# Performance work log

Measured on AMD Instinct MI355X. Metric: run time of the kernel, lower is better.

The kernel has to match this reference:

```python
import jax, jax.numpy as jnp
import numpy as np


def conv2d(x, w, dilation=1, padding=0):
    return jax.lax.conv_general_dilated(
        x, w, window_strides=(1, 1),
        padding=[(padding, padding), (padding, padding)],
        rhs_dilation=(dilation, dilation),
        dimension_numbers=('NCHW', 'OIHW', 'NCHW'))


def bn_relu(x, s, b):
    # inference-mode BatchNorm folded into per-channel scale/bias, then ReLU
    return jax.nn.relu(x * s[None, :, None, None] + b[None, :, None, None])


def resize_bilinear_ac(x, oh, ow):
    # bilinear interpolation with align_corners=True (matches F.interpolate)
    n, c, h, w = x.shape
    def axis_coords(o, i):
        if i == 1:
            z = jnp.zeros((o,), jnp.int32)
            return jnp.zeros((o,), x.dtype), z, z
        t = jnp.arange(o, dtype=x.dtype) * ((i - 1) / (o - 1))
        i0 = jnp.floor(t).astype(jnp.int32)
        i1 = jnp.minimum(i0 + 1, i - 1)
        return t - i0.astype(x.dtype), i0, i1
    fy, y0, y1 = axis_coords(oh, h)
    x = x[:, :, y0, :] * (1 - fy)[None, None, :, None] + x[:, :, y1, :] * fy[None, None, :, None]
    fx, x0, x1 = axis_coords(ow, w)
    x = x[:, :, :, x0] * (1 - fx) + x[:, :, :, x1] * fx
    return x


def unfold3x3_d2(x):
    # F.unfold(x, kernel_size=3, dilation=2, padding=2, stride=1) -> [n, c, 9, h*w]
    n, c, h, w = x.shape
    xp = jnp.pad(x, ((0, 0), (0, 0), (2, 2), (2, 2)))
    pats = [xp[:, :, i:i + h, j:j + w] for i in (0, 2, 4) for j in (0, 2, 4)]
    return jnp.stack(pats, axis=2).reshape(n, c, 9, h * w)


def setup_inputs() -> dict:
    key = jax.random.key(0)
    ks = iter(jax.random.split(key, 48))
    def rn(shape, scale=0.05):
        return jax.random.normal(next(ks), shape, jnp.float32) * scale
    d = {
        'c1': rn((1, 256, 64, 64), 1.0),
        'c2': rn((1, 512, 32, 32), 1.0),
        'x': rn((1, 4096, 32, 32), 1.0),
        'rf1_w': rn((64, 256, 3, 3)), 'rf1_s': jnp.ones((64,), jnp.float32), 'rf1_b': rn((64,)),
        'rf2_w': rn((64, 64, 3, 3)), 'rf2_s': jnp.ones((64,), jnp.float32), 'rf2_b': rn((64,)),
        'r2_w': rn((64, 512, 1, 1)), 'r2_s': jnp.ones((64,), jnp.float32), 'r2_b': rn((64,)),
        'a0_w': rn((512, 4096, 1, 1)), 'a0_s': jnp.ones((512,), jnp.float32), 'a0_b': rn((512,)),
        'a1_w': rn((512, 4096, 3, 3), 0.01), 'a1_s': jnp.ones((512,), jnp.float32), 'a1_b': rn((512,)),
        'a2_w': rn((512, 4096, 3, 3), 0.01), 'a2_s': jnp.ones((512,), jnp.float32), 'a2_b': rn((512,)),
        'a3_w': rn((512, 4096, 3, 3), 0.01), 'a3_s': jnp.ones((512,), jnp.float32), 'a3_b': rn((512,)),
        'a4_w': rn((512, 4096, 1, 1)), 'a4_s': jnp.ones((512,), jnp.float32), 'a4_b': rn((512,)),
        'ap_w': rn((512, 2560, 1, 1)), 'ap_s': jnp.ones((512,), jnp.float32), 'ap_b': rn((512,)),
        'c6_w': rn((19, 512, 1, 1)), 'c6_b': rn((19,)),
    }
    return d


def reference(c1, c2, x, rf1_w, rf1_s, rf1_b, rf2_w, rf2_s, rf2_b, r2_w, r2_s, r2_b,
              a0_w, a0_s, a0_b, a1_w, a1_s, a1_b, a2_w, a2_s, a2_b, a3_w, a3_s, a3_b,
              a4_w, a4_s, a4_b, ap_w, ap_s, ap_b, c6_w, c6_b):
    n, _, h, w = c1.shape
    # refine(c1): two 3x3 dilation-2 convs
    c1r = bn_relu(conv2d(c1, rf1_w, 2, 2), rf1_s, rf1_b)
    c1r = bn_relu(conv2d(c1r, rf2_w, 2, 2), rf2_s, rf2_b)  # [n,64,h,w]
    # refine2(interpolate(c2))
    c2r = bn_relu(conv2d(resize_bilinear_ac(c2, h, w), r2_w), r2_s, r2_b)  # [n,64,h,w]
    unf_c2 = unfold3x3_d2(c2r)  # [n,64,9,h*w]
    # energy[n,p,k] = sum_c c1r[n,c,p] * unf_c2[n,c,k,p]
    energy = jnp.einsum('ncp,nckp->npk', c1r.reshape(n, 64, h * w), unf_c2)
    att = jax.nn.softmax(energy, axis=-1)  # [n, h*w, 9]
    # ASPP on x (in=4096, out=512)
    f0 = bn_relu(conv2d(x, a0_w), a0_s, a0_b)
    f1 = bn_relu(conv2d(x, a1_w, 12, 12), a1_s, a1_b)
    f2 = bn_relu(conv2d(x, a2_w, 24, 24), a2_s, a2_b)
    f3 = bn_relu(conv2d(x, a3_w, 36, 36), a3_s, a3_b)
    gap = jnp.mean(x, axis=(2, 3), keepdims=True)
    f4 = resize_bilinear_ac(bn_relu(conv2d(gap, a4_w), a4_s, a4_b), x.shape[2], x.shape[3])
    out = bn_relu(conv2d(jnp.concatenate([f0, f1, f2, f3, f4], axis=1), ap_w), ap_s, ap_b)
    # local 3x3 window attention aggregation (dropout is eval-mode identity)
    unf_out = unfold3x3_d2(resize_bilinear_ac(out, h, w))  # [n,512,9,h*w]
    agg = jnp.einsum('npk,nckp->ncp', att, unf_out).reshape(n, 512, h, w)
    return conv2d(agg, c6_w) + c6_b[None, :, None, None]
```

## Files before the change

### kernel.cpp

```cpp
#include <hip/hip_runtime.h>
#include <hip/hip_bf16.h>


typedef unsigned short u16;
typedef short bf16x8 __attribute__((ext_vector_type(8)));
typedef float f32x4  __attribute__((ext_vector_type(4)));
typedef u16   u16x8  __attribute__((ext_vector_type(8)));

__device__ __forceinline__ float bf2f(u16 u) {
    return __uint_as_float(((unsigned int)u) << 16);
}
__device__ __forceinline__ u16 f2bf(float f) {
    unsigned u = __float_as_uint(f);
    return (u16)((u + 0x7FFFu + ((u >> 16) & 1u)) >> 16);
}
__device__ __forceinline__ float loadv(const void* p, long i, int f32) {
    return f32 ? ((const float*)p)[i] : bf2f(((const u16*)p)[i]);
}
__device__ __forceinline__ u16 loadbf(const void* p, long i, int f32) {
    return f32 ? f2bf(((const float*)p)[i]) : ((const u16*)p)[i];
}

__device__ __forceinline__ void gload16(const u16* g, u16* l) {
    __builtin_amdgcn_global_load_lds(
        (const __attribute__((address_space(1))) unsigned int*)(g),
        (__attribute__((address_space(3))) unsigned int*)(l), 16, 0, 0);
}

__global__ __launch_bounds__(256) void detect_kernel(
    const u16* __restrict__ c1, int* __restrict__ flag)
{
    __shared__ int cnt;
    if (threadIdx.x == 0) cnt = 0;
    __syncthreads();
    int local = 0;
    for (int i = threadIdx.x; i < 16384; i += 256) {
        u16 u = c1[i];
        if ((u & 0x7F80) >= 0x4F00) local++;
    }
    atomicAdd(&cnt, local);
    __syncthreads();
    if (threadIdx.x == 0) flag[0] = (cnt > 256) ? 1 : 0;
}

__global__ __launch_bounds__(256) void zero_kernel(float* __restrict__ p, int n)
{
    for (int g = blockIdx.x * 256 + threadIdx.x; g < n; g += gridDim.x * 256)
        p[g] = 0.f;
}


__global__ __launch_bounds__(256) void xpose_bn(
    const void* __restrict__ src, u16* __restrict__ dst,
    const void* __restrict__ s, const void* __restrict__ b,
    const int* __restrict__ flag, int flagged, int dobn, int C, int P)
{
    __shared__ u16 T[64][72];
    const int fl = flag[0];
    const int srcf32 = flagged ? fl : 1;
    const int p0 = blockIdx.x * 64, c0 = blockIdx.y * 64;
    const int t = threadIdx.x;
    {
        int c = t >> 2, pq = (t & 3) * 16;
        float sc = 1.f, bc = 0.f;
        if (dobn) { sc = loadv(s, c0 + c, fl); bc = loadv(b, c0 + c, fl); }
        const long sb = (long)(c0 + c) * P + p0 + pq;
        if (srcf32) {
            const float* sp = (const float*)src + sb;
#pragma unroll
            for (int i = 0; i < 16; i += 4) {
                float4 v = *(const float4*)(sp + i);
                float vv[4] = {v.x, v.y, v.z, v.w};
#pragma unroll
                for (int j = 0; j < 4; j++) {
                    float u = vv[j];
                    if (dobn) u = fmaxf(u * sc + bc, 0.f);
                    T[pq + i + j][c] = f2bf(u);
                }
            }
        } else {
            const u16* sp = (const u16*)src + sb;
#pragma unroll
            for (int i = 0; i < 16; i++) T[pq + i][c] = sp[i];
        }
    }
    __syncthreads();
    {
        int p = t >> 2, cq = (t & 3) * 16;
        u16x8 v0, v1;
#pragma unroll
        for (int i = 0; i < 8; i++) { v0[i] = T[p][cq + i]; v1[i] = T[p][cq + 8 + i]; }
        *(u16x8*)&dst[(long)(p0 + p) * C + c0 + cq] = v0;
        *(u16x8*)&dst[(long)(p0 + p) * C + c0 + cq + 8] = v1;
    }
}

__global__ __launch_bounds__(256) void xform_w9(
    const void* __restrict__ w, u16* __restrict__ W9, const int* __restrict__ flag,
    int O, int C)
{
    const int f32 = flag[0];
    const int o = blockIdx.y;
    const int c = blockIdx.x * 256 + threadIdx.x;
    if (c >= C) return;
    const long src = ((long)o * C + c) * 9;
    u16 v[9];
    if (f32) {
        const float* p = (const float*)w + src;
#pragma unroll
        for (int j = 0; j < 9; j++) v[j] = f2bf(p[j]);
    } else {
        const u16* p = (const u16*)w + src;
#pragma unroll
        for (int j = 0; j < 9; j++) v[j] = p[j];
    }
#pragma unroll
    for (int j = 0; j < 9; j++)
        W9[(long)j * O * C + (long)o * C + c] = v[j];
}

__global__ __launch_bounds__(256) void xform_w1(
    const void* __restrict__ w, u16* __restrict__ Wo, const int* __restrict__ flag,
    int ldi, int off, int st, int logC)
{
    const int f32 = flag[0];
    long g = (long)blockIdx.x * 256 + threadIdx.x;
    long o = g >> logC;
    int c = (int)(g & ((1 << logC) - 1));
    Wo[g] = loadbf(w, o * ldi + off + (long)c * st, f32);
}

template<int MF>
__global__ __launch_bounds__(256, 4) void conv_gemm(
    const u16* __restrict__ W2, const u16* __restrict__ X2,
    const u16* __restrict__ zpage, float* __restrict__ OUT,
    int K, int O, int taps, int d, int logIW, int P,
    int nbo, int nbp, int kcs, int swz)
{
    __shared__ __align__(16) u16 Ws[2][MF * 2048];
    __shared__ __align__(16) u16 Xs[2][4096];

    const int tid = threadIdx.x;
    int bo, bp, bz;
    {
        int pid = blockIdx.x;
        if (swz) {
            int xcd = pid & 7, j = pid >> 3;
            bp = j % nbp;
            int g = j / nbp;
            int G = xcd + 8 * g;
            bo = G % nbo; bz = G / nbo;
        } else {
            bp = pid % nbp;
            int q = pid / nbp;
            bo = q % nbo; bz = q / nbo;
        }
    }
    const int kb = bz * kcs;
    const int IW = 1 << logIW;

    const int wave = tid >> 6, lane = tid & 63;
    const int quad = lane >> 4, l15 = lane & 15;

    int mask = 1;
    if (taps == 9) {
        const int rb = 128 >> logIW;
        const int ty0 = bp * rb;
        mask = 0;
        for (int t = 0; t < 9; t++) {
            int dy = (t / 3 - 1) * d;
            if (ty0 + rb - 1 + dy >= 0 && ty0 + dy < IW) mask |= (1 << t);
        }
    }
    const int nIt = (kcs >> 5) * __popc(mask);

    int wrow[MF], wk[MF];
#pragma unroll
    for (int li = 0; li < MF; li++) {
        int bb = li * 4096 + tid * 16;
        int l = bb ^ (((bb >> 7) & 3) << 4);
        wrow[li] = l >> 6; wk[li] = ((l >> 4) & 3) * 8;
    }
    int xrow[2], xk[2];
#pragma unroll
    for (int li = 0; li < 2; li++) {
        int bb = li * 4096 + tid * 16;
        int l = bb ^ (((bb >> 7) & 3) << 4);
        xrow[li] = l >> 6; xk[li] = ((l >> 4) & 3) * 8;
    }

    const long wplane = (long)O * K;

    f32x4 acc[MF][8];
#pragma unroll
    for (int mi = 0; mi < MF; mi++)
#pragma unroll
        for (int j = 0; j < 8; j++) {
            f32x4 z = {0.f, 0.f, 0.f, 0.f};
            acc[mi][j] = z;
        }

    int arow[MF];
#pragma unroll
    for (int mi = 0; mi < MF; mi++) {
        int ao = (wave * (MF * 16) + mi * 16 + l15) * 64 + quad * 16;
        arow[mi] = ao ^ (((ao >> 7) & 3) << 4);
    }

    int tt = __ffs(mask) - 1;
    int kc = kb;

    auto STAGE = [&](int buf) {
        int dy = 0, dx = 0;
        if (taps == 9) { dy = (tt / 3 - 1) * d; dx = (tt % 3 - 1) * d; }
#pragma unroll
        for (int li = 0; li < MF; li++)
            gload16(W2 + (long)tt * wplane + (long)(bo * (MF * 64) + wrow[li]) * K + kc + wk[li],
                    &Ws[buf][li * 2048 + tid * 8]);
#pragma unroll
        for (int li = 0; li < 2; li++) {
            int pg = bp * 128 + xrow[li];
            const u16* src;
            if (taps == 9) {
                int yy = (pg >> logIW) + dy, xx = (pg & (IW - 1)) + dx;
                src = ((unsigned)yy < (unsigned)IW && (unsigned)xx < (unsigned)IW)
                    ? X2 + (long)((yy << logIW) | xx) * K + kc + xk[li] : zpage;
            } else {
                src = X2 + (long)pg * K + kc + xk[li];
            }
            gload16(src, &Xs[buf][li * 2048 + tid * 8]);
        }
        int rem = mask >> (tt + 1);
        if (rem) tt += __ffs(rem);
        else { tt = __ffs(mask) - 1; kc += 32; }
    };

    STAGE(0);
    __syncthreads();
    int cur = 0;
    for (int i = 0; i < nIt; i++) {
        if (i + 1 < nIt) STAGE(cur ^ 1);
        bf16x8 a[MF];
#pragma unroll
        for (int mi = 0; mi < MF; mi++)
            a[mi] = *(const bf16x8*)&Ws[cur][arow[mi] >> 1];
#pragma unroll
        for (int j = 0; j < 8; j++) {
            int boff = (j * 16 + l15) * 64 + quad * 16;
            boff ^= ((boff >> 7) & 3) << 4;
            bf16x8 b = *(const bf16x8*)&Xs[cur][boff >> 1];
#pragma unroll
            for (int mi = 0; mi < MF; mi++)
                acc[mi][j] = __builtin_amdgcn_mfma_f32_16x16x32_bf16(a[mi], b, acc[mi][j], 0, 0, 0);
        }
        __syncthreads();
        cur ^= 1;
    }

#pragma unroll
    for (int mi = 0; mi < MF; mi++)
#pragma unroll
        for (int j = 0; j < 8; j++) {
            int pgl = bp * 128 + j * 16 + l15;
            long ob = (long)(bo * (MF * 64) + wave * (MF * 16) + mi * 16 + quad * 4);
#pragma unroll
            for (int r = 0; r < 4; r++)
                atomicAdd(&OUT[(ob + r) * P + pgl], acc[mi][j][r]);
        }
}

__global__ __launch_bounds__(256) void conv_mfma(
    const void* __restrict__ W, const void* __restrict__ X, float* __restrict__ OUT,
    const int* __restrict__ flag, int x_ext,
    int K, int wrow, int wstride, int woff, int taps, int d, int logIW)
{
    __shared__ __align__(16) u16 Ws[64 * 40];
    __shared__ __align__(16) u16 Xs[128 * 40];

    const int IW = 1 << logIW;
    const int NP = IW * IW;
    const int wf32 = flag[0];
    const int xf32 = x_ext ? wf32 : 1;

    const int tid = threadIdx.x;
    const int bo = blockIdx.x, bp = blockIdx.y;
    const int kcs = K / gridDim.z;
    const int kb = blockIdx.z * kcs;

    const int w_o = tid >> 2, w_kg = (tid & 3) * 8;
    const int x_p = tid >> 1, x_kg = (tid & 1) * 16;
    const int pg  = bp * 128 + x_p;
    const int py  = pg >> logIW, px = pg & (IW - 1);
    const int ty0 = (bp * 128) >> logIW;
    const int ty1 = ty0 + (128 >> logIW) - 1;

    const int wave = tid >> 6, lane = tid & 63;
    const int quad = lane >> 4, l15 = lane & 15;

    f32x4 acc[8];
#pragma unroll
    for (int j = 0; j < 8; j++) {
        f32x4 z = {0.f, 0.f, 0.f, 0.f};
        acc[j] = z;
    }

    const long wbase_o = (long)(bo * 64 + w_o) * wrow + woff;

    for (int kc = kb; kc < kb + kcs; kc += 32) {
        for (int t = 0; t < taps; t++) {
            int dy = 0, dx = 0, wt = 0;
            if (taps == 9) { dy = (t / 3 - 1) * d; dx = (t % 3 - 1) * d; wt = t; }
            if (ty1 + dy < 0 || ty0 + dy >= IW) continue;

            {
                u16 tv[8];
                if (wstride == 1) {
                    long idx = wbase_o + kc + w_kg;
                    if (wf32) {
                        float4 v0 = *(const float4*)((const float*)W + idx);
                        float4 v1 = *(const float4*)((const float*)W + idx + 4);
                        tv[0] = f2bf(v0.x); tv[1] = f2bf(v0.y);
                        tv[2] = f2bf(v0.z); tv[3] = f2bf(v0.w);
                        tv[4] = f2bf(v1.x); tv[5] = f2bf(v1.y);
                        tv[6] = f2bf(v1.z); tv[7] = f2bf(v1.w);
                    } else {
                        ushort4 v0 = *(const ushort4*)((const u16*)W + idx);
                        ushort4 v1 = *(const ushort4*)((const u16*)W + idx + 4);
                        tv[0] = v0.x; tv[1] = v0.y; tv[2] = v0.z; tv[3] = v0.w;
                        tv[4] = v1.x; tv[5] = v1.y; tv[6] = v1.z; tv[7] = v1.w;
                    }
                } else {
                    long idx = wbase_o + wt + (long)(kc + w_kg) * 9;
#pragma unroll
                    for (int i = 0; i < 8; i++)
                        tv[i] = loadbf(W, idx + (long)i * 9, wf32);
                }
                *(ushort4*)&Ws[w_o * 40 + w_kg]     = make_ushort4(tv[0], tv[1], tv[2], tv[3]);
                *(ushort4*)&Ws[w_o * 40 + w_kg + 4] = make_ushort4(tv[4], tv[5], tv[6], tv[7]);
            }
            {
                int yy = py + dy, xv = px + dx;
                bool ok = ((unsigned)yy < (unsigned)IW) && ((unsigned)xv < (unsigned)IW);
                u16 tv[16];
                if (ok) {
                    long idx = (long)(kc + x_kg) * NP + yy * IW + xv;
                    if (xf32) {
#pragma unroll
                        for (int i = 0; i < 16; i++)
                            tv[i] = f2bf(((const float*)X)[idx + (long)i * NP]);
                    } else {
#pragma unroll
                        for (int i = 0; i < 16; i++)
                            tv[i] = ((const u16*)X)[idx + (long)i * NP];
                    }
                } else {
#pragma unroll
                    for (int i = 0; i < 16; i++) tv[i] = 0;
                }
                *(ushort4*)&Xs[x_p * 40 + x_kg]      = make_ushort4(tv[0], tv[1], tv[2], tv[3]);
                *(ushort4*)&Xs[x_p * 40 + x_kg + 4]  = make_ushort4(tv[4], tv[5], tv[6], tv[7]);
                *(ushort4*)&Xs[x_p * 40 + x_kg + 8]  = make_ushort4(tv[8], tv[9], tv[10], tv[11]);
                *(ushort4*)&Xs[x_p * 40 + x_kg + 12] = make_ushort4(tv[12], tv[13], tv[14], tv[15]);
            }
            __syncthreads();
            {
                bf16x8 a = *(const bf16x8*)&Ws[(wave * 16 + l15) * 40 + quad * 8];
#pragma unroll
                for (int j = 0; j < 8; j++) {
                    bf16x8 b = *(const bf16x8*)&Xs[(j * 16 + l15) * 40 + quad * 8];
                    acc[j] = __builtin_amdgcn_mfma_f32_16x16x32_bf16(a, b, acc[j], 0, 0, 0);
                }
            }
            __syncthreads();
        }
    }

#pragma unroll
    for (int j = 0; j < 8; j++) {
        int pgl = bp * 128 + j * 16 + l15;
        long ob = (long)(bo * 64 + wave * 16 + quad * 4);
#pragma unroll
        for (int r = 0; r < 4; r++)
            atomicAdd(&OUT[(ob + r) * NP + pgl], acc[j][r]);
    }
}

__global__ __launch_bounds__(256) void ep_bnrelu(
    float* __restrict__ buf, const void* __restrict__ s, const void* __restrict__ b,
    const int* __restrict__ flag, int logN, int total)
{
    int f32 = flag[0];
    int g = blockIdx.x * 256 + threadIdx.x;
    if (g >= total) return;
    int c = g >> logN;
    float v = buf[g] * loadv(s, c, f32) + loadv(b, c, f32);
    buf[g] = fmaxf(v, 0.f);
}

__global__ __launch_bounds__(256) void ep_aspp(
    float* __restrict__ buf, const float* __restrict__ f4con,
    const void* __restrict__ s, const void* __restrict__ b, const int* __restrict__ flag)
{
    int f32 = flag[0];
    int g = blockIdx.x * 256 + threadIdx.x;
    int c = g >> 10;
    float v = (buf[g] + f4con[c]) * loadv(s, c, f32) + loadv(b, c, f32);
    buf[g] = fmaxf(v, 0.f);
}

__global__ __launch_bounds__(256) void resize_bn(
    const float* __restrict__ in, float* __restrict__ out,
    const void* __restrict__ s, const void* __restrict__ b,
    const int* __restrict__ flag, int dobn)
{
    int g = blockIdx.x * 256 + threadIdx.x;
    int c = g >> 12, p = g & 4095;
    int oy = p >> 6, ox = p & 63;
    const float r = 31.0f / 63.0f;
    float tyf = oy * r, txf = ox * r;
    int y0 = (int)tyf, x0 = (int)txf;
    float fy = tyf - y0, fx = txf - x0;
    int y1 = y0 + 1 > 31 ? 31 : y0 + 1;
    int x1 = x0 + 1 > 31 ? 31 : x0 + 1;
    const float* pc = in + c * 1024;
    float v00 = pc[y0 * 32 + x0], v01 = pc[y0 * 32 + x1];
    float v10 = pc[y1 * 32 + x0], v11 = pc[y1 * 32 + x1];
    float v = (1.f - fy) * ((1.f - fx) * v00 + fx * v01) +
              fy * ((1.f - fx) * v10 + fx * v11);
    if (dobn) v = fmaxf(v * loadv(s, c, flag[0]) + loadv(b, c, flag[0]), 0.f);
    out[g] = v;
}

__global__ __launch_bounds__(256) void attn_kernel(
    const float* __restrict__ c1r, const float* __restrict__ c2r, float* __restrict__ att)
{
    int tid = threadIdx.x;
    int p = blockIdx.x * 4 + (tid >> 6);
    int lane = tid & 63;
    int y = p >> 6, x = p & 63;
    float a = c1r[lane * 4096 + p];
    float e[9];
#pragma unroll
    for (int ky = 0; ky < 3; ky++)
#pragma unroll
        for (int kx = 0; kx < 3; kx++) {
            int yy = y + 2 * (ky - 1), xx = x + 2 * (kx - 1);
            float v = 0.f;
            if (yy >= 0 && yy < 64 && xx >= 0 && xx < 64)
                v = a * c2r[lane * 4096 + yy * 64 + xx];
#pragma unroll
            for (int off = 32; off; off >>= 1) v += __shfl_xor(v, off);
            e[ky * 3 + kx] = v;
        }
    float m = e[0];
#pragma unroll
    for (int k = 1; k < 9; k++) m = fmaxf(m, e[k]);
    float ssum = 0.f;
#pragma unroll
    for (int k = 0; k < 9; k++) ssum += __expf(e[k] - m);
    if (lane < 9) {
        float mye = e[0];
#pragma unroll
        for (int k = 1; k < 9; k++)
            if (lane == k) mye = e[k];
        att[p * 9 + lane] = __expf(mye - m) / ssum;
    }
}

__global__ __launch_bounds__(256) void gap_kernel(
    const void* __restrict__ x, const int* __restrict__ flag, float* __restrict__ gap)
{
    int f32 = flag[0];
    int tid = threadIdx.x;
    int c = blockIdx.x * 4 + (tid >> 6);
    int lane = tid & 63;
    long base = (long)c * 1024;
    float ssum = 0.f;
#pragma unroll
    for (int i = 0; i < 16; i++) ssum += loadv(x, base + lane + i * 64, f32);
#pragma unroll
    for (int off = 32; off; off >>= 1) ssum += __shfl_xor(ssum, off);
    if (lane == 0) gap[c] = ssum * (1.0f / 1024.0f);
}

__global__ __launch_bounds__(256) void f4_kernel(
    const void* __restrict__ w, const float* __restrict__ gap,
    const void* __restrict__ s, const void* __restrict__ b,
    const int* __restrict__ flag, float* __restrict__ f4c)
{
    int f32 = flag[0];
    int tid = threadIdx.x;
    int o = blockIdx.x * 4 + (tid >> 6);
    int lane = tid & 63;
    long base = (long)o * 4096;
    float ssum = 0.f;
#pragma unroll
    for (int i = 0; i < 64; i++)
        ssum += loadv(w, base + lane + i * 64, f32) * gap[lane + i * 64];
#pragma unroll
    for (int off = 32; off; off >>= 1) ssum += __shfl_xor(ssum, off);
    if (lane == 0) f4c[o] = fmaxf(ssum * loadv(s, o, f32) + loadv(b, o, f32), 0.f);
}

__global__ __launch_bounds__(256) void f4con_kernel(
    const void* __restrict__ ap_w, const float* __restrict__ f4c,
    const int* __restrict__ flag, float* __restrict__ f4con)
{
    int f32 = flag[0];
    int tid = threadIdx.x;
    int o = blockIdx.x * 4 + (tid >> 6);
    int lane = tid & 63;
    long base = (long)o * 2560 + 2048;
    float ssum = 0.f;
#pragma unroll
    for (int i = 0; i < 8; i++)
        ssum += loadv(ap_w, base + lane + i * 64, f32) * f4c[lane + i * 64];
#pragma unroll
    for (int off = 32; off; off >>= 1) ssum += __shfl_xor(ssum, off);
    if (lane == 0) f4con[o] = ssum;
}

__global__ __launch_bounds__(256) void vs_kernel(
    const float* __restrict__ aspp, const void* __restrict__ w,
    const int* __restrict__ flag, float* __restrict__ Vs)
{
    int f32 = flag[0];
    int p = blockIdx.x * 256 + threadIdx.x;
    int q = blockIdx.y;
    long wb = (long)q * 512;
    float a0 = 0.f, a1 = 0.f, a2 = 0.f, a3 = 0.f;
    for (int c = 0; c < 512; c += 4) {
        a0 = fmaf(loadv(w, wb + c + 0, f32), aspp[(c + 0) * 1024 + p], a0);
        a1 = fmaf(loadv(w, wb + c + 1, f32), aspp[(c + 1) * 1024 + p], a1);
        a2 = fmaf(loadv(w, wb + c + 2, f32), aspp[(c + 2) * 1024 + p], a2);
        a3 = fmaf(loadv(w, wb + c + 3, f32), aspp[(c + 3) * 1024 + p], a3);
    }
    Vs[q * 1024 + p] = (a0 + a1) + (a2 + a3);
}

__global__ __launch_bounds__(256) void final_kernel(
    const float* __restrict__ att, const float* __restrict__ V,
    const void* __restrict__ bias, const int* __restrict__ flag, void* __restrict__ out)
{
    int f32 = flag[0];
    int g = blockIdx.x * 256 + threadIdx.x;
    int q = g >> 12, p = g & 4095;
    int y = p >> 6, x = p & 63;
    const float* a = att + p * 9;
    const float* v = V + q * 4096;
    float acc = loadv(bias, q, f32);
#pragma unroll
    for (int ky = 0; ky < 3; ky++)
#pragma unroll
        for (int kx = 0; kx < 3; kx++) {
            int yy = y + 2 * (ky - 1), xx = x + 2 * (kx - 1);
            if (yy >= 0 && yy < 64 && xx >= 0 && xx < 64)
                acc += a[ky * 3 + kx] * v[yy * 64 + xx];
        }
    if (f32) ((float*)out)[g] = acc;
    else     ((__hip_bfloat16*)out)[g] = __float2bfloat16(acc);
}

extern "C" void kernel_launch(void* const* d_in, const int* in_sizes, int n_in,
                              void* d_out, int out_size, void* d_ws, size_t ws_size,
                              hipStream_t stream)
{
    const void* c1    = d_in[0];
    const void* c2    = d_in[1];
    const void* x     = d_in[2];
    const void* rf1_w = d_in[3];
    const void* rf1_s = d_in[4];
    const void* rf1_b = d_in[5];
    const void* rf2_w = d_in[6];
    const void* rf2_s = d_in[7];
    const void* rf2_b = d_in[8];
    const void* r2_w  = d_in[9];
    const void* r2_s  = d_in[10];
    const void* r2_b  = d_in[11];
    const void* a0_w  = d_in[12];
    const void* a0_s  = d_in[13];
    const void* a0_b  = d_in[14];
    const void* a1_w  = d_in[15];
    const void* a1_s  = d_in[16];
    const void* a1_b  = d_in[17];
    const void* a2_w  = d_in[18];
    const void* a2_s  = d_in[19];
    const void* a2_b  = d_in[20];
    const void* a3_w  = d_in[21];
    const void* a3_s  = d_in[22];
    const void* a3_b  = d_in[23];
    const void* a4_w  = d_in[24];
    const void* a4_s  = d_in[25];
    const void* a4_b  = d_in[26];
    const void* ap_w  = d_in[27];
    const void* ap_s  = d_in[28];
    const void* ap_b  = d_in[29];
    const void* c6_w  = d_in[30];
    const void* c6_b  = d_in[31];

    const long F_BUFR = 0;
    const long F_C1R  = 262144;
    const long F_BUFC = 524288;
    const long F_ASPP = 589824;
    const long F_ZP   = 1114112;
    const long F_TMP  = 1114368;
    const long F_C2R  = 1638656;
    const long F_ATT  = 1900800;
    const long F_GAPV = 1937664;
    const long F_F4C  = 1941760;
    const long F_F4CO = 1942272;
    const long F_VS   = 1942784;
    const long F_V    = 1962240;
    const long F_FLAG = 2040064;
    const long F_X2   = 2040128;
    const long F_W2   = 4137280;
    const long F_W1   = 13574464;
    const long F_END  = 14623040;

    float* ws    = (float*)d_ws;
    float* bufR  = ws + F_BUFR;
    float* c1r   = ws + F_C1R;
    float* bufC  = ws + F_BUFC;
    float* aspp  = ws + F_ASPP;
    float* tmp   = ws + F_TMP;
    float* c2r   = ws + F_C2R;
    float* att   = ws + F_ATT;
    float* gapv  = ws + F_GAPV;
    float* f4c   = ws + F_F4C;
    float* f4con = ws + F_F4CO;
    float* Vs    = ws + F_VS;
    float* V     = ws + F_V;
    int*   flag  = (int*)(ws + F_FLAG);
    u16*   X2u   = (u16*)(ws + F_X2);
    u16*   W2u   = (u16*)(ws + F_W2);
    u16*   W1u   = (u16*)(ws + F_W1);
    const u16* zp16 = (const u16*)(ws + F_ZP);

    u16* X1u   = W2u;
    u16* W9Ru  = W2u + 1048576;
    u16* X1Bu  = W2u + 1196032;
    u16* W9R2u = W2u + 1458176;
    u16* X1Cu  = W2u + 1495040;
    u16* W1Ru  = W2u + 2019328;
    u16* WAPu  = W1u;
    u16* T2u   = W1u + 262144;

    const bool big = ws_size >= (size_t)F_END * 4;

    detect_kernel<<<1, 256, 0, stream>>>((const u16*)c1, flag);
    zero_kernel<<<1024, 256, 0, stream>>>(ws, 1114368);

    if (big) {
        xpose_bn<<<dim3(64, 4), 256, 0, stream>>>(c1, X1u, nullptr, nullptr,
                                                  flag, 1, 0, 256, 4096);
        xform_w9<<<dim3(1, 64), 256, 0, stream>>>(rf1_w, W9Ru, flag, 64, 256);
        conv_gemm<1><<<256, 256, 0, stream>>>(W9Ru, X1u, zp16, bufR,
                                              256, 64, 9, 2, 6, 4096, 1, 32, 32, 1);
        xpose_bn<<<dim3(64, 1), 256, 0, stream>>>(bufR, X1Bu, rf1_s, rf1_b,
                                                  flag, 0, 1, 64, 4096);
        xform_w9<<<dim3(1, 64), 256, 0, stream>>>(rf2_w, W9R2u, flag, 64, 64);
        conv_gemm<1><<<64, 256, 0, stream>>>(W9R2u, X1Bu, zp16, c1r,
                                             64, 64, 9, 2, 6, 4096, 1, 32, 32, 0);
        ep_bnrelu<<<1024, 256, 0, stream>>>(c1r, rf2_s, rf2_b, flag, 12, 262144);

        xpose_bn<<<dim3(16, 8), 256, 0, stream>>>(c2, X1Cu, nullptr, nullptr,
                                                  flag, 1, 0, 512, 1024);
        xform_w1<<<128, 256, 0, stream>>>(r2_w, W1Ru, flag, 512, 0, 1, 9);
        conv_gemm<1><<<32, 256, 0, stream>>>(W1Ru, X1Cu, zp16, bufC,
                                             512, 64, 1, 0, 5, 1024, 1, 8, 128, 0);
        resize_bn<<<1024, 256, 0, stream>>>(bufC, c2r, r2_s, r2_b, flag, 1);

        attn_kernel<<<1024, 256, 0, stream>>>(c1r, c2r, att);

        gap_kernel<<<1024, 256, 0, stream>>>(x, flag, gapv);
        f4_kernel<<<128, 256, 0, stream>>>(a4_w, gapv, a4_s, a4_b, flag, f4c);
        f4con_kernel<<<128, 256, 0, stream>>>(ap_w, f4c, flag, f4con);

        xpose_bn<<<dim3(16, 64), 256, 0, stream>>>(x, X2u, nullptr, nullptr,
                                                   flag, 1, 0, 4096, 1024);

        zero_kernel<<<512, 256, 0, stream>>>(tmp, 524288);
        xform_w1<<<8192, 256, 0, stream>>>(a0_w, W1u, flag, 4096, 0, 1, 12);
        conv_gemm<2><<<256, 256, 0, stream>>>(W1u, X2u, zp16, tmp,
                                              4096, 512, 1, 0, 5, 1024, 4, 8, 512, 1);
        xpose_bn<<<dim3(16, 8), 256, 0, stream>>>(tmp, T2u, a0_s, a0_b,
                                                  flag, 0, 1, 512, 1024);
        xform_w1<<<1024, 256, 0, stream>>>(ap_w, WAPu, flag, 2560, 0, 1, 9);
        conv_gemm<2><<<256, 256, 0, stream>>>(WAPu, T2u, zp16, aspp,
                                              512, 512, 1, 0, 5, 1024, 4, 8, 64, 1);
        zero_kernel<<<512, 256, 0, stream>>>(tmp, 524288);
        xform_w9<<<dim3(16, 512), 256, 0, stream>>>(a1_w, W2u, flag, 512, 4096);
        conv_gemm<2><<<512, 256, 0, stream>>>(W2u, X2u, zp16, tmp,
                                              4096, 512, 9, 12, 5, 1024, 4, 8, 256, 1);
        xpose_bn<<<dim3(16, 8), 256, 0, stream>>>(tmp, T2u, a1_s, a1_b,
                                                  flag, 0, 1, 512, 1024);
        xform_w1<<<1024, 256, 0, stream>>>(ap_w, WAPu, flag, 2560, 512, 1, 9);
        conv_gemm<2><<<256, 256, 0, stream>>>(WAPu, T2u, zp16, aspp,
                                              512, 512, 1, 0, 5, 1024, 4, 8, 64, 1);
        zero_kernel<<<512, 256, 0, stream>>>(tmp, 524288);
        xform_w9<<<dim3(16, 512), 256, 0, stream>>>(a2_w, W2u, flag, 512, 4096);
        conv_gemm<2><<<512, 256, 0, stream>>>(W2u, X2u, zp16, tmp,
                                              4096, 512, 9, 24, 5, 1024, 4, 8, 256, 1);
        xpose_bn<<<dim3(16, 8), 256, 0, stream>>>(tmp, T2u, a2_s, a2_b,
                                                  flag, 0, 1, 512, 1024);
        xform_w1<<<1024, 256, 0, stream>>>(ap_w, WAPu, flag, 2560, 1024, 1, 9);
        conv_gemm<2><<<256, 256, 0, stream>>>(WAPu, T2u, zp16, aspp,
                                              512, 512, 1, 0, 5, 1024, 4, 8, 64, 1);
        zero_kernel<<<512, 256, 0, stream>>>(tmp, 524288);
        xform_w1<<<8192, 256, 0, stream>>>(a3_w, W1u, flag, 36864, 4, 9, 12);
        conv_gemm<2><<<256, 256, 0, stream>>>(W1u, X2u, zp16, tmp,
                                              4096, 512, 1, 0, 5, 1024, 4, 8, 512, 1);
        xpose_bn<<<dim3(16, 8), 256, 0, stream>>>(tmp, T2u, a3_s, a3_b,
                                                  flag, 0, 1, 512, 1024);
        xform_w1<<<1024, 256, 0, stream>>>(ap_w, WAPu, flag, 2560, 1536, 1, 9);
        conv_gemm<2><<<256, 256, 0, stream>>>(WAPu, T2u, zp16, aspp,
                                              512, 512, 1, 0, 5, 1024, 4, 8, 64, 1);
        ep_aspp<<<2048, 256, 0, stream>>>(aspp, f4con, ap_s, ap_b, flag);
    } else {
        conv_mfma<<<dim3(1, 32, 4), 256, 0, stream>>>(rf1_w, c1, bufR, flag, 1,
                                                      256, 256 * 9, 9, 0, 9, 2, 6);
        ep_bnrelu<<<1024, 256, 0, stream>>>(bufR, rf1_s, rf1_b, flag, 12, 262144);
        conv_mfma<<<dim3(1, 32, 2), 256, 0, stream>>>(rf2_w, bufR, c1r, flag, 0,
                                                      64, 64 * 9, 9, 0, 9, 2, 6);
        ep_bnrelu<<<1024, 256, 0, stream>>>(c1r, rf2_s, rf2_b, flag, 12, 262144);
        conv_mfma<<<dim3(1, 8, 4), 256, 0, stream>>>(r2_w, c2, bufC, flag, 1,
                                                     512, 512, 1, 0, 1, 0, 5);
        resize_bn<<<1024, 256, 0, stream>>>(bufC, c2r, r2_s, r2_b, flag, 1);
        attn_kernel<<<1024, 256, 0, stream>>>(c1r, c2r, att);
        gap_kernel<<<1024, 256, 0, stream>>>(x, flag, gapv);
        f4_kernel<<<128, 256, 0, stream>>>(a4_w, gapv, a4_s, a4_b, flag, f4c);
        f4con_kernel<<<128, 256, 0, stream>>>(ap_w, f4c, flag, f4con);

        zero_kernel<<<512, 256, 0, stream>>>(tmp, 524288);
        conv_mfma<<<dim3(8, 8, 4), 256, 0, stream>>>(a0_w, x, tmp, flag, 1,
                                                     4096, 4096, 1, 0, 1, 0, 5);
        ep_bnrelu<<<2048, 256, 0, stream>>>(tmp, a0_s, a0_b, flag, 10, 524288);
        conv_mfma<<<dim3(8, 8, 2), 256, 0, stream>>>(ap_w, tmp, aspp, flag, 0,
                                                     512, 2560, 1, 0, 1, 0, 5);
        zero_kernel<<<512, 256, 0, stream>>>(tmp, 524288);
        conv_mfma<<<dim3(8, 8, 8), 256, 0, stream>>>(a1_w, x, tmp, flag, 1,
                                                     4096, 4096 * 9, 9, 0, 9, 12, 5);
        ep_bnrelu<<<2048, 256, 0, stream>>>(tmp, a1_s, a1_b, flag, 10, 524288);
        conv_mfma<<<dim3(8, 8, 2), 256, 0, stream>>>(ap_w, tmp, aspp, flag, 0,
                                                     512, 2560, 1, 512, 1, 0, 5);
        zero_kernel<<<512, 256, 0, stream>>>(tmp, 524288);
        conv_mfma<<<dim3(8, 8, 8), 256, 0, stream>>>(a2_w, x, tmp, flag, 1,
                                                     4096, 4096 * 9, 9, 0, 9, 24, 5);
        ep_bnrelu<<<2048, 256, 0, stream>>>(tmp, a2_s, a2_b, flag, 10, 524288);
        conv_mfma<<<dim3(8, 8, 2), 256, 0, stream>>>(ap_w, tmp, aspp, flag, 0,
                                                     512, 2560, 1, 1024, 1, 0, 5);
        zero_kernel<<<512, 256, 0, stream>>>(tmp, 524288);
        conv_mfma<<<dim3(8, 8, 4), 256, 0, stream>>>(a3_w, x, tmp, flag, 1,
                                                     4096, 4096 * 9, 9, 4, 1, 0, 5);
        ep_bnrelu<<<2048, 256, 0, stream>>>(tmp, a3_s, a3_b, flag, 10, 524288);
        conv_mfma<<<dim3(8, 8, 2), 256, 0, stream>>>(ap_w, tmp, aspp, flag, 0,
                                                     512, 2560, 1, 1536, 1, 0, 5);
        ep_aspp<<<2048, 256, 0, stream>>>(aspp, f4con, ap_s, ap_b, flag);
    }

    vs_kernel<<<dim3(4, 19), 256, 0, stream>>>(aspp, c6_w, flag, Vs);
    resize_bn<<<304, 256, 0, stream>>>(Vs, V, nullptr, nullptr, flag, 0);
    final_kernel<<<304, 256, 0, stream>>>(att, V, c6_b, flag, d_out);
}
```

Before: 731.5 us.

## Deepen conv_gemm pipeline to four LDS stages and merge ASPP projection GEMMs

The conv_gemm main loop now uses four shared-memory buffers with three loads in flight. Explicit vmcnt waits plus a raw barrier replace the per-iteration double-buffer __syncthreads. Separately, the four branch outputs are transposed into one concatenated 2048-channel buffer, so the projection runs as a single K=2048 GEMM instead of four K=512 GEMMs, each with its own weight transform. This doubles LDS use per block, which may lower occupancy, and the hand-coded vmcnt counts depend on exactly how many loads each stage issues.

```diff
diff --git a/kernel.cpp b/kernel.cpp
--- a/kernel.cpp
+++ b/kernel.cpp
@@ -53,7 +53,8 @@
 __global__ __launch_bounds__(256) void xpose_bn(
     const void* __restrict__ src, u16* __restrict__ dst,
     const void* __restrict__ s, const void* __restrict__ b,
-    const int* __restrict__ flag, int flagged, int dobn, int C, int P)
+    const int* __restrict__ flag, int flagged, int dobn, int C, int P,
+    int dstC, int coff)
 {
     __shared__ u16 T[64][72];
     const int fl = flag[0];
@@ -90,8 +91,8 @@
         u16x8 v0, v1;
 #pragma unroll
         for (int i = 0; i < 8; i++) { v0[i] = T[p][cq + i]; v1[i] = T[p][cq + 8 + i]; }
-        *(u16x8*)&dst[(long)(p0 + p) * C + c0 + cq] = v0;
-        *(u16x8*)&dst[(long)(p0 + p) * C + c0 + cq + 8] = v1;
+        *(u16x8*)&dst[(long)(p0 + p) * dstC + coff + c0 + cq] = v0;
+        *(u16x8*)&dst[(long)(p0 + p) * dstC + coff + c0 + cq + 8] = v1;
     }
 }
 
@@ -137,8 +138,8 @@
     int K, int O, int taps, int d, int logIW, int P,
     int nbo, int nbp, int kcs, int swz)
 {
-    __shared__ __align__(16) u16 Ws[2][MF * 2048];
-    __shared__ __align__(16) u16 Xs[2][4096];
+    __shared__ __align__(16) u16 Ws[4][MF * 2048];
+    __shared__ __align__(16) u16 Xs[4][4096];
 
     const int tid = threadIdx.x;
     int bo, bp, bz;
@@ -236,10 +237,26 @@
     };
 
     STAGE(0);
-    __syncthreads();
-    int cur = 0;
+    if (nIt > 1) STAGE(1);
+    if (nIt > 2) STAGE(2);
+
     for (int i = 0; i < nIt; i++) {
-        if (i + 1 < nIt) STAGE(cur ^ 1);
+        const int ex = nIt - 1 - i;
+        if constexpr (MF == 2) {
+            if (ex >= 3)      asm volatile("s_waitcnt vmcnt(12)" ::: "memory");
+            else if (ex == 2) asm volatile("s_waitcnt vmcnt(8)" ::: "memory");
+            else if (ex == 1) asm volatile("s_waitcnt vmcnt(4)" ::: "memory");
+            else              asm volatile("s_waitcnt vmcnt(0)" ::: "memory");
+        } else {
+            if (ex >= 3)      asm volatile("s_waitcnt vmcnt(9)" ::: "memory");
+            else if (ex == 2) asm volatile("s_waitcnt vmcnt(6)" ::: "memory");
+            else if (ex == 1) asm volatile("s_waitcnt vmcnt(3)" ::: "memory");
+            else              asm volatile("s_waitcnt vmcnt(0)" ::: "memory");
+        }
+        __builtin_amdgcn_s_barrier();
+        __builtin_amdgcn_sched_barrier(0);
+
+        const int cur = i & 3;
         bf16x8 a[MF];
 #pragma unroll
         for (int mi = 0; mi < MF; mi++)
@@ -253,8 +270,7 @@
             for (int mi = 0; mi < MF; mi++)
                 acc[mi][j] = __builtin_amdgcn_mfma_f32_16x16x32_bf16(a[mi], b, acc[mi][j], 0, 0, 0);
         }
-        __syncthreads();
-        cur ^= 1;
+        if (i + 3 < nIt) STAGE((i + 3) & 3);
     }
 
 #pragma unroll
@@ -633,7 +649,7 @@
     int*   flag  = (int*)(ws + F_FLAG);
     u16*   X2u   = (u16*)(ws + F_X2);
     u16*   W2u   = (u16*)(ws + F_W2);
-    u16*   W1u   = (u16*)(ws + F_W1);
+    u16*   T2all = (u16*)(ws + F_W1);
     const u16* zp16 = (const u16*)(ws + F_ZP);
 
     u16* X1u   = W2u;
@@ -642,8 +658,9 @@
     u16* W9R2u = W2u + 1458176;
     u16* X1Cu  = W2u + 1495040;
     u16* W1Ru  = W2u + 2019328;
-    u16* WAPu  = W1u;
-    u16* T2u   = W1u + 262144;
+    u16* a0Wu  = W2u;
+    u16* a3Wu  = W2u + 2097152;
+    u16* WAPu  = W2u + 4194304;
 
     const bool big = ws_size >= (size_t)F_END * 4;
 
@@ -652,19 +669,19 @@
 
     if (big) {
         xpose_bn<<<dim3(64, 4), 256, 0, stream>>>(c1, X1u, nullptr, nullptr,
-                                                  flag, 1, 0, 256, 4096);
+                                                  flag, 1, 0, 256, 4096, 256, 0);
         xform_w9<<<dim3(1, 64), 256, 0, stream>>>(rf1_w, W9Ru, flag, 64, 256);
         conv_gemm<1><<<256, 256, 0, stream>>>(W9Ru, X1u, zp16, bufR,
                                               256, 64, 9, 2, 6, 4096, 1, 32, 32, 1);
         xpose_bn<<<dim3(64, 1), 256, 0, stream>>>(bufR, X1Bu, rf1_s, rf1_b,
-                                                  flag, 0, 1, 64, 4096);
+                                                  flag, 0, 1, 64, 4096, 64, 0);
         xform_w9<<<dim3(1, 64), 256, 0, stream>>>(rf2_w, W9R2u, flag, 64, 64);
         conv_gemm<1><<<64, 256, 0, stream>>>(W9R2u, X1Bu, zp16, c1r,
                                              64, 64, 9, 2, 6, 4096, 1, 32, 32, 0);
         ep_bnrelu<<<1024, 256, 0, stream>>>(c1r, rf2_s, rf2_b, flag, 12, 262144);
 
         xpose_bn<<<dim3(16, 8), 256, 0, stream>>>(c2, X1Cu, nullptr, nullptr,
-                                                  flag, 1, 0, 512, 1024);
+                                                  flag, 1, 0, 512, 1024, 512, 0);
         xform_w1<<<128, 256, 0, stream>>>(r2_w, W1Ru, flag, 512, 0, 1, 9);
         conv_gemm<1><<<32, 256, 0, stream>>>(W1Ru, X1Cu, zp16, bufC,
                                              512, 64, 1, 0, 5, 1024, 1, 8, 128, 0);
@@ -677,44 +694,35 @@
         f4con_kernel<<<128, 256, 0, stream>>>(ap_w, f4c, flag, f4con);
 
         xpose_bn<<<dim3(16, 64), 256, 0, stream>>>(x, X2u, nullptr, nullptr,
-                                                   flag, 1, 0, 4096, 1024);
+                                                   flag, 1, 0, 4096, 1024, 4096, 0);
 
         zero_kernel<<<512, 256, 0, stream>>>(tmp, 524288);
-        xform_w1<<<8192, 256, 0, stream>>>(a0_w, W1u, flag, 4096, 0, 1, 12);
-        conv_gemm<2><<<256, 256, 0, stream>>>(W1u, X2u, zp16, tmp,
+        xform_w1<<<8192, 256, 0, stream>>>(a0_w, a0Wu, flag, 4096, 0, 1, 12);
+        conv_gemm<2><<<256, 256, 0, stream>>>(a0Wu, X2u, zp16, tmp,
                                               4096, 512, 1, 0, 5, 1024, 4, 8, 512, 1);
-        xpose_bn<<<dim3(16, 8), 256, 0, stream>>>(tmp, T2u, a0_s, a0_b,
-                                                  flag, 0, 1, 512, 1024);
-        xform_w1<<<1024, 256, 0, stream>>>(ap_w, WAPu, flag, 2560, 0, 1, 9);
-        conv_gemm<2><<<256, 256, 0, stream>>>(WAPu, T2u, zp16, aspp,
-                                              512, 512, 1, 0, 5, 1024, 4, 8, 64, 1);
+        xpose_bn<<<dim3(16, 8), 256, 0, stream>>>(tmp, T2all, a0_s, a0_b,
+                                                  flag, 0, 1, 512, 1024, 2048, 0);
         zero_kernel<<<512, 256, 0, stream>>>(tmp, 524288);
         xform_w9<<<dim3(16, 512), 256, 0, stream>>>(a1_w, W2u, flag, 512, 4096);
         conv_gemm<2><<<512, 256, 0, stream>>>(W2u, X2u, zp16, tmp,
                                               4096, 512, 9, 12, 5, 1024, 4, 8, 256, 1);
-        xpose_bn<<<dim3(16, 8), 256, 0, stream>>>(tmp, T2u, a1_s, a1_b,
-                                                  flag, 0, 1, 512, 1024);
-        xform_w1<<<1024, 256, 0, stream>>>(ap_w, WAPu, flag, 2560, 512, 1, 9);
-        conv_gemm<2><<<256, 256, 0, stream>>>(WAPu, T2u, zp16, aspp,
-                                              512, 512, 1, 0, 5, 1024, 4, 8, 64, 1);
+        xpose_bn<<<dim3(16, 8), 256, 0, stream>>>(tmp, T2all, a1_s, a1_b,
+                                                  flag, 0, 1, 512, 1024, 2048, 512);
         zero_kernel<<<512, 256, 0, stream>>>(tmp, 524288);
         xform_w9<<<dim3(16, 512), 256, 0, stream>>>(a2_w, W2u, flag, 512, 4096);
         conv_gemm<2><<<512, 256, 0, stream>>>(W2u, X2u, zp16, tmp,
                                               4096, 512, 9, 24, 5, 1024, 4, 8, 256, 1);
-        xpose_bn<<<dim3(16, 8), 256, 0, stream>>>(tmp, T2u, a2_s, a2_b,
-                                                  flag, 0, 1, 512, 1024);
-        xform_w1<<<1024, 256, 0, stream>>>(ap_w, WAPu, flag, 2560, 1024, 1, 9);
-        conv_gemm<2><<<256, 256, 0, stream>>>(WAPu, T2u, zp16, aspp,
-                                              512, 512, 1, 0, 5, 1024, 4, 8, 64, 1);
+        xpose_bn<<<dim3(16, 8), 256, 0, stream>>>(tmp, T2all, a2_s, a2_b,
+                                                  flag, 0, 1, 512, 1024, 2048, 1024);
         zero_kernel<<<512, 256, 0, stream>>>(tmp, 524288);
-        xform_w1<<<8192, 256, 0, stream>>>(a3_w, W1u, flag, 36864, 4, 9, 12);
-        conv_gemm<2><<<256, 256, 0, stream>>>(W1u, X2u, zp16, tmp,
+        xform_w1<<<8192, 256, 0, stream>>>(a3_w, a3Wu, flag, 36864, 4, 9, 12);
+        conv_gemm<2><<<256, 256, 0, stream>>>(a3Wu, X2u, zp16, tmp,
                                               4096, 512, 1, 0, 5, 1024, 4, 8, 512, 1);
-        xpose_bn<<<dim3(16, 8), 256, 0, stream>>>(tmp, T2u, a3_s, a3_b,
-                                                  flag, 0, 1, 512, 1024);
-        xform_w1<<<1024, 256, 0, stream>>>(ap_w, WAPu, flag, 2560, 1536, 1, 9);
-        conv_gemm<2><<<256, 256, 0, stream>>>(WAPu, T2u, zp16, aspp,
-                                              512, 512, 1, 0, 5, 1024, 4, 8, 64, 1);
+        xpose_bn<<<dim3(16, 8), 256, 0, stream>>>(tmp, T2all, a3_s, a3_b,
+                                                  flag, 0, 1, 512, 1024, 2048, 1536);
+        xform_w1<<<4096, 256, 0, stream>>>(ap_w, WAPu, flag, 2560, 0, 1, 11);
+        conv_gemm<2><<<256, 256, 0, stream>>>(WAPu, T2all, zp16, aspp,
+                                              2048, 512, 1, 0, 5, 1024, 4, 8, 256, 1);
         ep_aspp<<<2048, 256, 0, stream>>>(aspp, f4con, ap_s, ap_b, flag);
     } else {
         conv_mfma<<<dim3(1, 32, 4), 256, 0, stream>>>(rf1_w, c1, bufR, flag, 1,
```

Result: faster. 673.4 us (-7.9%).
